# Kernel optimization log

Hardware: AMD Instinct MI355X
Metric: run time of the kernel (lower is better)

The kernel has to match this reference:

```python
import jax, jax.numpy as jnp
import numpy as np

NEG_INF = jnp.finfo(jnp.float32).min


def _continual_mask(attach_test_after, Q, K, test_num, chunk_size):
    """Boolean allowed-mask [B, 1, Q, K] replicating get_continual_mask +
    the per-batch test-query/train-key override in forward()."""
    k_train = K - test_num * chunk_size
    q_train = Q - test_num * chunk_size
    qi = jnp.arange(Q)[:, None]          # [Q,1]
    kj = jnp.arange(K)[None, :]          # [1,K]
    # base causal mask with diagonal offset K-Q (train queries)
    base = kj <= qi + (K - Q)            # [Q,K]
    # block-diagonal tril for test-query / test-key region
    dq = qi - q_train                    # local test row (negative for train rows, unused there)
    dk = kj - k_train
    block = (kj >= k_train) & (dk <= dq) & ((dk // chunk_size) == (dq // chunk_size))
    # per-batch: test query in chunk n may see train keys <= attach_test_after[b, n]
    chunk_idx = jnp.clip(dq[:, 0], 0, None) // chunk_size          # [Q]
    att = attach_test_after[:, chunk_idx]                          # [B,Q]
    train_key_allowed = kj[None, :, :] <= att[:, :, None]          # [B,Q,K]
    allowed = jnp.where(qi < q_train, base[None],
                        jnp.where(kj[None] < k_train, train_key_allowed, block[None]))
    return allowed[:, None]              # [B,1,Q,K]


def setup_inputs() -> dict:
    key = jax.random.key(0)
    k1, k2, k3, k4 = jax.random.split(key, 4)
    B, L, H, D = 4, 2048, 8, 64
    test_num, train_len = 64, 1536
    return {
        "queries": jax.random.normal(k1, (B, L, H, D), dtype=jnp.float32),
        "keys": jax.random.normal(k2, (B, L, H, D), dtype=jnp.float32),
        "values": jax.random.normal(k3, (B, L, H, D), dtype=jnp.float32),
        "attach_test_after": jax.random.randint(k4, (B, test_num), 0, train_len).astype(jnp.int64),
        "train_len": train_len,
    }


def reference(queries, keys, values, attach_test_after, train_len):
    B, Lq, H, Dqk = queries.shape
    test_num = attach_test_after.shape[1]
    chunk_size = (Lq - train_len) // test_num
    q = jnp.transpose(queries, (0, 2, 1, 3))   # [B,H,Lq,D]
    k = jnp.transpose(keys, (0, 2, 1, 3))      # [B,H,Lk,D]
    v = jnp.transpose(values, (0, 2, 1, 3))    # [B,H,Lk,Dv]
    Lk = k.shape[2]
    # vanilla path: scaled QK^T + continual mask + softmax + AV
    logits = jnp.einsum('bhmd,bhnd->bhmn', q, k) / jnp.sqrt(jnp.float32(Dqk))
    allowed = _continual_mask(attach_test_after, Lq, Lk, test_num, chunk_size)
    logits = jnp.where(allowed, logits, NEG_INF)
    attn = jax.nn.softmax(logits, axis=-1)
    out = jnp.einsum('bhmn,bhnd->bhmd', attn, v)
    return out.transpose(0, 2, 1, 3).reshape(B, Lq, H * v.shape[-1])  # b l (h d)
```

## Files before the change

kernel.cpp:

```cpp
#include <hip/hip_runtime.h>
#include <hip/hip_bf16.h>

typedef __bf16 bf16_t;
typedef __bf16 bf16x8 __attribute__((ext_vector_type(8)));
typedef float  f32x4  __attribute__((ext_vector_type(4)));

#define MFMA16(a, b, c) __builtin_amdgcn_mfma_f32_16x16x32_bf16((a), (b), (c), 0, 0, 0)

constexpr int Bc = 4, Lc = 2048, Hc = 8, Dc = 64;
constexpr int HD = Hc * Dc;
constexpr int TRAINc = 1536;
constexpr int ROWS_BLK = 128;
constexpr int KT = 64;

constexpr int PREPK_BLOCKS = (int)((size_t)Bc * Lc * Hc * Dc / 8 / 256);

__global__ void prep_fused(const float* __restrict__ K, bf16_t* __restrict__ Kb,
                           const float* __restrict__ V, bf16_t* __restrict__ Vt) {
  __shared__ bf16_t T[64][64];
  const int t = (int)threadIdx.x;

  if ((int)blockIdx.x < PREPK_BLOCKS) {
    size_t g = ((size_t)blockIdx.x * 256 + t) * 8;
    float4 a = *(const float4*)(K + g);
    float4 b = *(const float4*)(K + g + 4);
    bf16x8 v;
    v[0] = (bf16_t)a.x; v[1] = (bf16_t)a.y; v[2] = (bf16_t)a.z; v[3] = (bf16_t)a.w;
    v[4] = (bf16_t)b.x; v[5] = (bf16_t)b.y; v[6] = (bf16_t)b.z; v[7] = (bf16_t)b.w;
    *(bf16x8*)(Kb + g) = v;
    return;
  }

  const int bid = (int)blockIdx.x - PREPK_BLOCKS;
  const int kt = bid & 31, h = (bid >> 5) & 7, b = bid >> 8;
  {
    int kl = t >> 2, dp = (t & 3) << 4;
    const float* s = V + ((size_t)(b * Lc + kt * 64 + kl) * Hc + h) * Dc + dp;
    bf16x8 v0, v1;
    float4 f;
    f = *(const float4*)(s);      v0[0]=(bf16_t)f.x; v0[1]=(bf16_t)f.y; v0[2]=(bf16_t)f.z; v0[3]=(bf16_t)f.w;
    f = *(const float4*)(s + 4);  v0[4]=(bf16_t)f.x; v0[5]=(bf16_t)f.y; v0[6]=(bf16_t)f.z; v0[7]=(bf16_t)f.w;
    f = *(const float4*)(s + 8);  v1[0]=(bf16_t)f.x; v1[1]=(bf16_t)f.y; v1[2]=(bf16_t)f.z; v1[3]=(bf16_t)f.w;
    f = *(const float4*)(s + 12); v1[4]=(bf16_t)f.x; v1[5]=(bf16_t)f.y; v1[6]=(bf16_t)f.z; v1[7]=(bf16_t)f.w;
    const int x = kl >> 3;
    const int c0 = dp >> 3;
    *(bf16x8*)&T[kl][(c0 ^ x) << 3]       = v0;
    *(bf16x8*)&T[kl][((c0 + 1) ^ x) << 3] = v1;
  }
  __syncthreads();
  {
    int d = t >> 2, kp = (t & 3) << 4;
    const int xa = kp >> 3;
    const int xb = xa + 1;
    const int lo = d & 7, hi = d >> 3;
    const int x0 = ((hi ^ xa) << 3) + lo;
    const int x1 = ((hi ^ xb) << 3) + lo;
    bf16x8 o0, o1;
#pragma unroll
    for (int i = 0; i < 8; ++i) { o0[i] = T[kp + i][x0]; o1[i] = T[kp + 8 + i][x1]; }
    bf16_t* dst = Vt + ((size_t)((b * Hc + h) * Dc + d)) * Lc + kt * 64 + kp;
    *(bf16x8*)dst = o0;
    *(bf16x8*)(dst + 8) = o1;
  }
}

static __device__ __forceinline__ void load16(const bf16_t* g, bf16_t* l) {
  __builtin_amdgcn_global_load_lds(
      (const __attribute__((address_space(1))) unsigned int*)g,
      (__attribute__((address_space(3))) unsigned int*)l, 16, 0, 0);
}

__global__ __launch_bounds__(512, 4)
void continual_attn(const float* __restrict__ Qg, const bf16_t* __restrict__ Kb,
                    const bf16_t* __restrict__ Vt, const int* __restrict__ ATT,
                    float* __restrict__ OUT)
{
  __shared__ __align__(16) bf16_t Klds[2][KT * 64];
  __shared__ __align__(16) bf16_t Vlds[2][Dc * KT];
  __shared__ __align__(16) bf16_t Plds[8][16 * 64];

  const int bid  = blockIdx.x;
  const int g    = bid >> 5;
  const int qblk = (g < 8) ? (15 - g) : (g - 8);
  const int h    = bid & 7;
  const int b    = (bid >> 3) & 3;
  const int q0   = qblk * ROWS_BLK;

  const int tid  = (int)threadIdx.x;
  const int wave = tid >> 6;
  const int lane = tid & 63;
  const int quad = lane >> 4;
  const int col  = lane & 15;
  const int qw   = q0 + wave * 16;

  const size_t bhQ = (size_t)b * Lc * HD + (size_t)h * Dc;

  const int kr = tid >> 3;
  const int sw = ((tid & 7) ^ (kr & 7)) << 3;
  const bf16_t* ksrc = Kb + bhQ + (size_t)kr * HD + sw;
  const bf16_t* vsrc = Vt + ((size_t)((b * Hc + h) * Dc + kr)) * Lc + sw;

  bf16x8 aq[2];
  {
    const float* qp = Qg + bhQ + (size_t)(qw + col) * HD + quad * 8;
    const float SC = 0.125f * 1.44269504f;
#pragma unroll
    for (int t = 0; t < 2; ++t) {
      float4 lo = *(const float4*)(qp + t * 32);
      float4 hi = *(const float4*)(qp + t * 32 + 4);
      bf16x8 v;
      v[0] = (bf16_t)(lo.x * SC); v[1] = (bf16_t)(lo.y * SC);
      v[2] = (bf16_t)(lo.z * SC); v[3] = (bf16_t)(lo.w * SC);
      v[4] = (bf16_t)(hi.x * SC); v[5] = (bf16_t)(hi.y * SC);
      v[6] = (bf16_t)(hi.z * SC); v[7] = (bf16_t)(hi.w * SC);
      aq[t] = v;
    }
  }

  const bool testblk = (q0 >= TRAINc);
  int kend[4], cstart[4], qir[4];
#pragma unroll
  for (int r = 0; r < 4; ++r) {
    int qi = qw + quad * 4 + r;
    qir[r] = qi;
    if (testblk) {
      kend[r]   = ATT[b * 64 + ((qi - TRAINc) >> 3)] + 1;
      cstart[r] = qi & ~7;
    } else {
      kend[r]   = qi + 1;
      cstart[r] = 0;
    }
  }

  int ntA, ndiag, kfull_end;
  if (testblk) {
    int c0 = (q0 - TRAINc) >> 3;
    int amax = 0, amin = 0x7fffffff;
#pragma unroll
    for (int i = 0; i < 16; ++i) {
      int a = ATT[b * 64 + c0 + i];
      amax = (a > amax) ? a : amax;
      amin = (a < amin) ? a : amin;
    }
    ntA = (amax >> 6) + 1;
    ndiag = 2;
    kfull_end = amin + 1;
  } else {
    ntA = 2 * qblk + 2;
    ndiag = 0;
    kfull_end = q0 + 1;
  }
  const int ntot = ntA + ndiag;

  float lsumL[4] = {0.f, 0.f, 0.f, 0.f};
  f32x4 o[4] = {{0,0,0,0},{0,0,0,0},{0,0,0,0},{0,0,0,0}};

  const int cA = ((quad ^ (col & 7)) << 3);
  const int c7 = col & 7;
  const int c8 = col >> 3;

  {
    load16(ksrc, Klds[0] + wave * 512);
    load16(vsrc, Vlds[0] + wave * 512);
  }

  for (int ti = 0; ti < ntot; ++ti) {
    const int buf = ti & 1;
    __syncthreads();

    if (ti + 1 < ntot) {
      const int kn = (ti + 1 < ntA) ? (ti + 1) * KT : q0 + (ti + 1 - ntA) * KT;
      load16(ksrc + (size_t)kn * HD, Klds[1 - buf] + wave * 512);
      load16(vsrc + kn,              Vlds[1 - buf] + wave * 512);
    }

    const bf16_t* kb = Klds[buf];
    const bf16_t* vbuf = Vlds[buf];
    const int k0 = (ti < ntA) ? ti * KT : q0 + (ti - ntA) * KT;

    f32x4 sf[4] = {{0,0,0,0},{0,0,0,0},{0,0,0,0},{0,0,0,0}};
    __builtin_amdgcn_s_setprio(1);
#pragma unroll
    for (int kg = 0; kg < 4; ++kg) {
      const bf16_t* krow = kb + (kg * 16 + col) * 64;
      bf16x8 k0f = *(const bf16x8*)(krow + cA);
      bf16x8 k1f = *(const bf16x8*)(krow + (cA ^ 32));
      sf[kg] = MFMA16(aq[0], k0f, sf[kg]);
      sf[kg] = MFMA16(aq[1], k1f, sf[kg]);
    }
    __builtin_amdgcn_s_setprio(0);

    const int mode = (ti >= ntA) ? 2 : ((k0 + KT <= kfull_end) ? 0 : 1);
    if (mode == 1) {
#pragma unroll
      for (int kg = 0; kg < 4; ++kg) {
        const int kgv = k0 + kg * 16 + col;
#pragma unroll
        for (int r = 0; r < 4; ++r)
          if (kgv >= kend[r]) sf[kg][r] = -1e30f;
      }
    } else if (mode == 2) {
#pragma unroll
      for (int kg = 0; kg < 4; ++kg) {
        const int kgv = k0 + kg * 16 + col;
#pragma unroll
        for (int r = 0; r < 4; ++r)
          if (kgv < cstart[r] || kgv > qir[r]) sf[kg][r] = -1e30f;
      }
    }

    bf16_t* pw = Plds[wave];
#pragma unroll
    for (int kg = 0; kg < 4; ++kg) {
#pragma unroll
      for (int r = 0; r < 4; ++r) {
        float p = __builtin_amdgcn_exp2f(sf[kg][r]);
        lsumL[r] += p;
        const int row = quad * 4 + r;
        pw[row * 64 + (((2 * kg + c8) ^ (row & 7)) << 3) + c7] = (bf16_t)p;
      }
    }
    bf16x8 pa0 = *(const bf16x8*)&pw[col * 64 + ((quad ^ c7) << 3)];
    bf16x8 pa1 = *(const bf16x8*)&pw[col * 64 + (((4 + quad) ^ c7) << 3)];

    __builtin_amdgcn_s_setprio(1);
#pragma unroll
    for (int t = 0; t < 4; ++t) {
      const bf16_t* vrow = vbuf + (t * 16 + col) * 64;
      bf16x8 v0 = *(const bf16x8*)(vrow + cA);
      bf16x8 v1 = *(const bf16x8*)(vrow + (cA ^ 32));
      o[t] = MFMA16(pa0, v0, o[t]);
      o[t] = MFMA16(pa1, v1, o[t]);
    }
    __builtin_amdgcn_s_setprio(0);
  }

#pragma unroll
  for (int r = 0; r < 4; ++r) {
    float rs = lsumL[r];
    rs += __shfl_xor(rs, 1);
    rs += __shfl_xor(rs, 2);
    rs += __shfl_xor(rs, 4);
    rs += __shfl_xor(rs, 8);
    float inv = 1.f / rs;
    int qi = qw + quad * 4 + r;
    float* op = OUT + ((size_t)b * Lc + qi) * HD + (size_t)h * Dc + col;
    op[0]  = o[0][r] * inv;
    op[16] = o[1][r] * inv;
    op[32] = o[2][r] * inv;
    op[48] = o[3][r] * inv;
  }
}

extern "C" void kernel_launch(void* const* d_in, const int* in_sizes, int n_in,
                              void* d_out, int out_size, void* d_ws, size_t ws_size,
                              hipStream_t stream) {
  const float* Q   = (const float*)d_in[0];
  const float* K   = (const float*)d_in[1];
  const float* V   = (const float*)d_in[2];
  const int*   ATT = (const int*)d_in[3];
  float* OUT = (float*)d_out;
  (void)in_sizes; (void)n_in; (void)out_size; (void)ws_size;

  const size_t NE = (size_t)Bc * Lc * Hc * Dc;
  bf16_t* Kb = (bf16_t*)d_ws;
  bf16_t* Vt = Kb + NE;

  prep_fused<<<dim3((unsigned)(PREPK_BLOCKS + Bc * Hc * (Lc / 64))), dim3(256), 0, stream>>>(K, Kb, V, Vt);
  continual_attn<<<dim3(Bc * Hc * (Lc / ROWS_BLK)), dim3(512), 0, stream>>>(Q, Kb, Vt, ATT, OUT);
}
```

Measured before the change: 133.1 us.

## Double key tile width to 128 with split K/V LDS halves

Raises the key/value tile from 64 to 128 keys per loop iteration. Each tile is loaded as two 64-key halves into LDS, with a new V-transpose addressing scheme, and softmax-probability writes plus PV MFMAs are processed in two halves. The aim is to halve the number of loop iterations, barriers and prefetch rounds per block. The cost is more register pressure from 8 score accumulators, and more wasted work on partially masked causal and diagonal tiles because of the coarser key granularity.

```diff
diff --git a/kernel.cpp b/kernel.cpp
--- a/kernel.cpp
+++ b/kernel.cpp
@@ -11,7 +11,7 @@
 constexpr int HD = Hc * Dc;
 constexpr int TRAINc = 1536;
 constexpr int ROWS_BLK = 128;
-constexpr int KT = 64;
+constexpr int KT = 128;
 
 constexpr int PREPK_BLOCKS = (int)((size_t)Bc * Lc * Hc * Dc / 8 / 256);
 
@@ -96,9 +96,13 @@
   const size_t bhQ = (size_t)b * Lc * HD + (size_t)h * Dc;
 
   const int kr = tid >> 3;
-  const int sw = ((tid & 7) ^ (kr & 7)) << 3;
-  const bf16_t* ksrc = Kb + bhQ + (size_t)kr * HD + sw;
-  const bf16_t* vsrc = Vt + ((size_t)((b * Hc + h) * Dc + kr)) * Lc + sw;
+  const bf16_t* ksrc = Kb + bhQ + (size_t)kr * HD + (((tid & 7) ^ (kr & 7)) << 3);
+  const int vd  = wave * 4 + (lane >> 4);
+  const int vhh = (lane >> 3) & 1;
+  const int vc  = lane & 7;
+  const bf16_t* vsrc = Vt + ((size_t)((b * Hc + h) * Dc + vd)) * Lc
+                         + vhh * 64 + ((vc ^ (vd & 7)) << 3);
+  const bf16_t* vsrc2 = vsrc + (size_t)32 * Lc;
 
   bf16x8 aq[2];
   {
@@ -142,11 +146,11 @@
       amax = (a > amax) ? a : amax;
       amin = (a < amin) ? a : amin;
     }
-    ntA = (amax >> 6) + 1;
-    ndiag = 2;
+    ntA = (amax >> 7) + 1;
+    ndiag = 1;
     kfull_end = amin + 1;
   } else {
-    ntA = 2 * qblk + 2;
+    ntA = qblk + 1;
     ndiag = 0;
     kfull_end = q0 + 1;
   }
@@ -160,8 +164,10 @@
   const int c8 = col >> 3;
 
   {
-    load16(ksrc, Klds[0] + wave * 512);
-    load16(vsrc, Vlds[0] + wave * 512);
+    load16(ksrc,                      Klds[0] + wave * 512);
+    load16(ksrc + (size_t)64 * HD,    Klds[0] + 4096 + wave * 512);
+    load16(vsrc,                      Vlds[0] + wave * 512);
+    load16(vsrc2,                     Vlds[0] + 4096 + wave * 512);
   }
 
   for (int ti = 0; ti < ntot; ++ti) {
@@ -169,19 +175,24 @@
     __syncthreads();
 
     if (ti + 1 < ntot) {
-      const int kn = (ti + 1 < ntA) ? (ti + 1) * KT : q0 + (ti + 1 - ntA) * KT;
-      load16(ksrc + (size_t)kn * HD, Klds[1 - buf] + wave * 512);
-      load16(vsrc + kn,              Vlds[1 - buf] + wave * 512);
+      const int kn = (ti + 1 < ntA) ? (ti + 1) * KT : q0;
+      bf16_t* kd = Klds[1 - buf];
+      bf16_t* vdl = Vlds[1 - buf];
+      load16(ksrc + (size_t)kn * HD,        kd + wave * 512);
+      load16(ksrc + (size_t)(kn + 64) * HD, kd + 4096 + wave * 512);
+      load16(vsrc + kn,                     vdl + wave * 512);
+      load16(vsrc2 + kn,                    vdl + 4096 + wave * 512);
     }
 
     const bf16_t* kb = Klds[buf];
     const bf16_t* vbuf = Vlds[buf];
-    const int k0 = (ti < ntA) ? ti * KT : q0 + (ti - ntA) * KT;
-
-    f32x4 sf[4] = {{0,0,0,0},{0,0,0,0},{0,0,0,0},{0,0,0,0}};
+    const int k0 = (ti < ntA) ? ti * KT : q0;
+
+    f32x4 sf[8] = {{0,0,0,0},{0,0,0,0},{0,0,0,0},{0,0,0,0},
+                   {0,0,0,0},{0,0,0,0},{0,0,0,0},{0,0,0,0}};
     __builtin_amdgcn_s_setprio(1);
 #pragma unroll
-    for (int kg = 0; kg < 4; ++kg) {
+    for (int kg = 0; kg < 8; ++kg) {
       const bf16_t* krow = kb + (kg * 16 + col) * 64;
       bf16x8 k0f = *(const bf16x8*)(krow + cA);
       bf16x8 k1f = *(const bf16x8*)(krow + (cA ^ 32));
@@ -193,7 +204,7 @@
     const int mode = (ti >= ntA) ? 2 : ((k0 + KT <= kfull_end) ? 0 : 1);
     if (mode == 1) {
 #pragma unroll
-      for (int kg = 0; kg < 4; ++kg) {
+      for (int kg = 0; kg < 8; ++kg) {
         const int kgv = k0 + kg * 16 + col;
 #pragma unroll
         for (int r = 0; r < 4; ++r)
@@ -201,7 +212,7 @@
       }
     } else if (mode == 2) {
 #pragma unroll
-      for (int kg = 0; kg < 4; ++kg) {
+      for (int kg = 0; kg < 8; ++kg) {
         const int kgv = k0 + kg * 16 + col;
 #pragma unroll
         for (int r = 0; r < 4; ++r)
@@ -211,28 +222,31 @@
 
     bf16_t* pw = Plds[wave];
 #pragma unroll
-    for (int kg = 0; kg < 4; ++kg) {
-#pragma unroll
-      for (int r = 0; r < 4; ++r) {
-        float p = __builtin_amdgcn_exp2f(sf[kg][r]);
-        lsumL[r] += p;
-        const int row = quad * 4 + r;
-        pw[row * 64 + (((2 * kg + c8) ^ (row & 7)) << 3) + c7] = (bf16_t)p;
-      }
-    }
-    bf16x8 pa0 = *(const bf16x8*)&pw[col * 64 + ((quad ^ c7) << 3)];
-    bf16x8 pa1 = *(const bf16x8*)&pw[col * 64 + (((4 + quad) ^ c7) << 3)];
-
-    __builtin_amdgcn_s_setprio(1);
-#pragma unroll
-    for (int t = 0; t < 4; ++t) {
-      const bf16_t* vrow = vbuf + (t * 16 + col) * 64;
-      bf16x8 v0 = *(const bf16x8*)(vrow + cA);
-      bf16x8 v1 = *(const bf16x8*)(vrow + (cA ^ 32));
-      o[t] = MFMA16(pa0, v0, o[t]);
-      o[t] = MFMA16(pa1, v1, o[t]);
-    }
-    __builtin_amdgcn_s_setprio(0);
+    for (int hh = 0; hh < 2; ++hh) {
+#pragma unroll
+      for (int kgl = 0; kgl < 4; ++kgl) {
+#pragma unroll
+        for (int r = 0; r < 4; ++r) {
+          float p = __builtin_amdgcn_exp2f(sf[hh * 4 + kgl][r]);
+          lsumL[r] += p;
+          const int row = quad * 4 + r;
+          pw[row * 64 + (((2 * kgl + c8) ^ (row & 7)) << 3) + c7] = (bf16_t)p;
+        }
+      }
+      bf16x8 pa0 = *(const bf16x8*)&pw[col * 64 + ((quad ^ c7) << 3)];
+      bf16x8 pa1 = *(const bf16x8*)&pw[col * 64 + (((4 + quad) ^ c7) << 3)];
+
+      __builtin_amdgcn_s_setprio(1);
+#pragma unroll
+      for (int t = 0; t < 4; ++t) {
+        const bf16_t* vrow = vbuf + (t * 16 + col) * 128 + hh * 64;
+        bf16x8 v0 = *(const bf16x8*)(vrow + cA);
+        bf16x8 v1 = *(const bf16x8*)(vrow + (cA ^ 32));
+        o[t] = MFMA16(pa0, v0, o[t]);
+        o[t] = MFMA16(pa1, v1, o[t]);
+      }
+      __builtin_amdgcn_s_setprio(0);
+    }
   }
 
 #pragma unroll
```

Result: slower. 140.6 us (+5.7%).

## Process 32 query rows per wave with 4 waves per block to reuse K/V fragments

Applied to the files above, without the earlier changes.

Each wave now handles two 16-row query groups instead of one, and blocks shrink from 8 to 4 waves while still covering 128 rows. Each K and V fragment read from LDS feeds two MFMAs, which halves LDS read traffic per FLOP, and each thread issues twice as many async global-to-LDS loads. The cost is roughly double the accumulator and score registers per wave and fewer waves per block to hide latency. Launch bounds change to 256 threads with min 2 blocks.

```diff
diff --git a/kernel.cpp b/kernel.cpp
--- a/kernel.cpp
+++ b/kernel.cpp
@@ -70,18 +70,18 @@
       (__attribute__((address_space(3))) unsigned int*)l, 16, 0, 0);
 }
 
-__global__ __launch_bounds__(512, 4)
+__global__ __launch_bounds__(256, 2)
 void continual_attn(const float* __restrict__ Qg, const bf16_t* __restrict__ Kb,
                     const bf16_t* __restrict__ Vt, const int* __restrict__ ATT,
                     float* __restrict__ OUT)
 {
   __shared__ __align__(16) bf16_t Klds[2][KT * 64];
   __shared__ __align__(16) bf16_t Vlds[2][Dc * KT];
-  __shared__ __align__(16) bf16_t Plds[8][16 * 64];
+  __shared__ __align__(16) bf16_t Plds[4][32 * 64];
 
   const int bid  = blockIdx.x;
-  const int g    = bid >> 5;
-  const int qblk = (g < 8) ? (15 - g) : (g - 8);
+  const int gg   = bid >> 5;
+  const int qblk = (gg < 8) ? (15 - gg) : (gg - 8);
   const int h    = bid & 7;
   const int b    = (bid >> 3) & 3;
   const int q0   = qblk * ROWS_BLK;
@@ -91,18 +91,20 @@
   const int lane = tid & 63;
   const int quad = lane >> 4;
   const int col  = lane & 15;
-  const int qw   = q0 + wave * 16;
+  const int qw0  = q0 + wave * 32;
 
   const size_t bhQ = (size_t)b * Lc * HD + (size_t)h * Dc;
 
   const int kr = tid >> 3;
   const int sw = ((tid & 7) ^ (kr & 7)) << 3;
-  const bf16_t* ksrc = Kb + bhQ + (size_t)kr * HD + sw;
-  const bf16_t* vsrc = Vt + ((size_t)((b * Hc + h) * Dc + kr)) * Lc + sw;
-
-  bf16x8 aq[2];
-  {
-    const float* qp = Qg + bhQ + (size_t)(qw + col) * HD + quad * 8;
+  const bf16_t* ksrcA = Kb + bhQ + (size_t)kr * HD + sw;
+  const bf16_t* vsrcA = Vt + ((size_t)((b * Hc + h) * Dc + kr)) * Lc + sw;
+  const bf16_t* vsrcB = vsrcA + (size_t)32 * Lc;
+
+  bf16x8 aq[2][2];
+#pragma unroll
+  for (int g = 0; g < 2; ++g) {
+    const float* qp = Qg + bhQ + (size_t)(qw0 + g * 16 + col) * HD + quad * 8;
     const float SC = 0.125f * 1.44269504f;
 #pragma unroll
     for (int t = 0; t < 2; ++t) {
@@ -113,24 +115,20 @@
       v[2] = (bf16_t)(lo.z * SC); v[3] = (bf16_t)(lo.w * SC);
       v[4] = (bf16_t)(hi.x * SC); v[5] = (bf16_t)(hi.y * SC);
       v[6] = (bf16_t)(hi.z * SC); v[7] = (bf16_t)(hi.w * SC);
-      aq[t] = v;
+      aq[g][t] = v;
     }
   }
 
   const bool testblk = (q0 >= TRAINc);
-  int kend[4], cstart[4], qir[4];
-#pragma unroll
-  for (int r = 0; r < 4; ++r) {
-    int qi = qw + quad * 4 + r;
-    qir[r] = qi;
-    if (testblk) {
-      kend[r]   = ATT[b * 64 + ((qi - TRAINc) >> 3)] + 1;
-      cstart[r] = qi & ~7;
-    } else {
-      kend[r]   = qi + 1;
-      cstart[r] = 0;
-    }
-  }
+  int kend[2][4], qir[2][4];
+#pragma unroll
+  for (int g = 0; g < 2; ++g)
+#pragma unroll
+    for (int r = 0; r < 4; ++r) {
+      int qi = qw0 + g * 16 + quad * 4 + r;
+      qir[g][r] = qi;
+      kend[g][r] = testblk ? (ATT[b * 64 + ((qi - TRAINc) >> 3)] + 1) : (qi + 1);
+    }
 
   int ntA, ndiag, kfull_end;
   if (testblk) {
@@ -152,16 +150,19 @@
   }
   const int ntot = ntA + ndiag;
 
-  float lsumL[4] = {0.f, 0.f, 0.f, 0.f};
-  f32x4 o[4] = {{0,0,0,0},{0,0,0,0},{0,0,0,0},{0,0,0,0}};
+  float lsumL[2][4] = {{0.f,0.f,0.f,0.f},{0.f,0.f,0.f,0.f}};
+  f32x4 o[2][4] = {{{0,0,0,0},{0,0,0,0},{0,0,0,0},{0,0,0,0}},
+                   {{0,0,0,0},{0,0,0,0},{0,0,0,0},{0,0,0,0}}};
 
   const int cA = ((quad ^ (col & 7)) << 3);
   const int c7 = col & 7;
   const int c8 = col >> 3;
 
   {
-    load16(ksrc, Klds[0] + wave * 512);
-    load16(vsrc, Vlds[0] + wave * 512);
+    load16(ksrcA,                    Klds[0] + wave * 512);
+    load16(ksrcA + (size_t)32 * HD,  Klds[0] + 2048 + wave * 512);
+    load16(vsrcA,                    Vlds[0] + wave * 512);
+    load16(vsrcB,                    Vlds[0] + 2048 + wave * 512);
   }
 
   for (int ti = 0; ti < ntot; ++ti) {
@@ -170,23 +171,31 @@
 
     if (ti + 1 < ntot) {
       const int kn = (ti + 1 < ntA) ? (ti + 1) * KT : q0 + (ti + 1 - ntA) * KT;
-      load16(ksrc + (size_t)kn * HD, Klds[1 - buf] + wave * 512);
-      load16(vsrc + kn,              Vlds[1 - buf] + wave * 512);
+      bf16_t* kd = Klds[1 - buf];
+      bf16_t* vd = Vlds[1 - buf];
+      load16(ksrcA + (size_t)kn * HD,        kd + wave * 512);
+      load16(ksrcA + (size_t)(kn + 32) * HD, kd + 2048 + wave * 512);
+      load16(vsrcA + kn,                     vd + wave * 512);
+      load16(vsrcB + kn,                     vd + 2048 + wave * 512);
     }
 
     const bf16_t* kb = Klds[buf];
     const bf16_t* vbuf = Vlds[buf];
     const int k0 = (ti < ntA) ? ti * KT : q0 + (ti - ntA) * KT;
 
-    f32x4 sf[4] = {{0,0,0,0},{0,0,0,0},{0,0,0,0},{0,0,0,0}};
+    f32x4 sf[2][4] = {{{0,0,0,0},{0,0,0,0},{0,0,0,0},{0,0,0,0}},
+                      {{0,0,0,0},{0,0,0,0},{0,0,0,0},{0,0,0,0}}};
     __builtin_amdgcn_s_setprio(1);
 #pragma unroll
     for (int kg = 0; kg < 4; ++kg) {
       const bf16_t* krow = kb + (kg * 16 + col) * 64;
       bf16x8 k0f = *(const bf16x8*)(krow + cA);
       bf16x8 k1f = *(const bf16x8*)(krow + (cA ^ 32));
-      sf[kg] = MFMA16(aq[0], k0f, sf[kg]);
-      sf[kg] = MFMA16(aq[1], k1f, sf[kg]);
+#pragma unroll
+      for (int g = 0; g < 2; ++g) {
+        sf[g][kg] = MFMA16(aq[g][0], k0f, sf[g][kg]);
+        sf[g][kg] = MFMA16(aq[g][1], k1f, sf[g][kg]);
+      }
     }
     __builtin_amdgcn_s_setprio(0);
 
@@ -196,32 +205,42 @@
       for (int kg = 0; kg < 4; ++kg) {
         const int kgv = k0 + kg * 16 + col;
 #pragma unroll
-        for (int r = 0; r < 4; ++r)
-          if (kgv >= kend[r]) sf[kg][r] = -1e30f;
+        for (int g = 0; g < 2; ++g)
+#pragma unroll
+          for (int r = 0; r < 4; ++r)
+            if (kgv >= kend[g][r]) sf[g][kg][r] = -1e30f;
       }
     } else if (mode == 2) {
 #pragma unroll
       for (int kg = 0; kg < 4; ++kg) {
         const int kgv = k0 + kg * 16 + col;
 #pragma unroll
-        for (int r = 0; r < 4; ++r)
-          if (kgv < cstart[r] || kgv > qir[r]) sf[kg][r] = -1e30f;
+        for (int g = 0; g < 2; ++g)
+#pragma unroll
+          for (int r = 0; r < 4; ++r)
+            if (kgv < (qir[g][r] & ~7) || kgv > qir[g][r]) sf[g][kg][r] = -1e30f;
       }
     }
 
     bf16_t* pw = Plds[wave];
 #pragma unroll
-    for (int kg = 0; kg < 4; ++kg) {
-#pragma unroll
-      for (int r = 0; r < 4; ++r) {
-        float p = __builtin_amdgcn_exp2f(sf[kg][r]);
-        lsumL[r] += p;
-        const int row = quad * 4 + r;
-        pw[row * 64 + (((2 * kg + c8) ^ (row & 7)) << 3) + c7] = (bf16_t)p;
-      }
-    }
-    bf16x8 pa0 = *(const bf16x8*)&pw[col * 64 + ((quad ^ c7) << 3)];
-    bf16x8 pa1 = *(const bf16x8*)&pw[col * 64 + (((4 + quad) ^ c7) << 3)];
+    for (int g = 0; g < 2; ++g)
+#pragma unroll
+      for (int kg = 0; kg < 4; ++kg)
+#pragma unroll
+        for (int r = 0; r < 4; ++r) {
+          float p = __builtin_amdgcn_exp2f(sf[g][kg][r]);
+          lsumL[g][r] += p;
+          const int row = g * 16 + quad * 4 + r;
+          pw[row * 64 + (((2 * kg + c8) ^ (row & 7)) << 3) + c7] = (bf16_t)p;
+        }
+
+    bf16x8 pa0[2], pa1[2];
+#pragma unroll
+    for (int g = 0; g < 2; ++g) {
+      pa0[g] = *(const bf16x8*)&pw[(g * 16 + col) * 64 + ((quad ^ c7) << 3)];
+      pa1[g] = *(const bf16x8*)&pw[(g * 16 + col) * 64 + (((4 + quad) ^ c7) << 3)];
+    }
 
     __builtin_amdgcn_s_setprio(1);
 #pragma unroll
@@ -229,27 +248,32 @@
       const bf16_t* vrow = vbuf + (t * 16 + col) * 64;
       bf16x8 v0 = *(const bf16x8*)(vrow + cA);
       bf16x8 v1 = *(const bf16x8*)(vrow + (cA ^ 32));
-      o[t] = MFMA16(pa0, v0, o[t]);
-      o[t] = MFMA16(pa1, v1, o[t]);
+#pragma unroll
+      for (int g = 0; g < 2; ++g) {
+        o[g][t] = MFMA16(pa0[g], v0, o[g][t]);
+        o[g][t] = MFMA16(pa1[g], v1, o[g][t]);
+      }
     }
     __builtin_amdgcn_s_setprio(0);
   }
 
 #pragma unroll
-  for (int r = 0; r < 4; ++r) {
-    float rs = lsumL[r];
-    rs += __shfl_xor(rs, 1);
-    rs += __shfl_xor(rs, 2);
-    rs += __shfl_xor(rs, 4);
-    rs += __shfl_xor(rs, 8);
-    float inv = 1.f / rs;
-    int qi = qw + quad * 4 + r;
-    float* op = OUT + ((size_t)b * Lc + qi) * HD + (size_t)h * Dc + col;
-    op[0]  = o[0][r] * inv;
-    op[16] = o[1][r] * inv;
-    op[32] = o[2][r] * inv;
-    op[48] = o[3][r] * inv;
-  }
+  for (int g = 0; g < 2; ++g)
+#pragma unroll
+    for (int r = 0; r < 4; ++r) {
+      float rs = lsumL[g][r];
+      rs += __shfl_xor(rs, 1);
+      rs += __shfl_xor(rs, 2);
+      rs += __shfl_xor(rs, 4);
+      rs += __shfl_xor(rs, 8);
+      float inv = 1.f / rs;
+      int qi = qw0 + g * 16 + quad * 4 + r;
+      float* op = OUT + ((size_t)b * Lc + qi) * HD + (size_t)h * Dc + col;
+      op[0]  = o[g][0][r] * inv;
+      op[16] = o[g][1][r] * inv;
+      op[32] = o[g][2][r] * inv;
+      op[48] = o[g][3][r] * inv;
+    }
 }
 
 extern "C" void kernel_launch(void* const* d_in, const int* in_sizes, int n_in,
@@ -267,5 +291,5 @@
   bf16_t* Vt = Kb + NE;
 
   prep_fused<<<dim3((unsigned)(PREPK_BLOCKS + Bc * Hc * (Lc / 64))), dim3(256), 0, stream>>>(K, Kb, V, Vt);
-  continual_attn<<<dim3(Bc * Hc * (Lc / ROWS_BLK)), dim3(512), 0, stream>>>(Q, Kb, Vt, ATT, OUT);
-}
+  continual_attn<<<dim3(Bc * Hc * (Lc / ROWS_BLK)), dim3(256), 0, stream>>>(Q, Kb, Vt, ATT, OUT);
+}
```

Result: slower. 139.3 us (+4.7%).
